# Kernel optimization log

Measured on AMD Instinct MI355X. Metric: run time of the kernel, lower is better.

## Reference

```python
import jax, jax.numpy as jnp
import numpy as np

D = 1024

def setup_inputs() -> dict:
    key = jax.random.key(0)
    ks = jax.random.split(key, 7)
    s = 1.0 / np.sqrt(D)
    x = jax.random.normal(ks[0], (4, 4096, D), dtype=jnp.float32)
    Wq = jax.random.uniform(ks[1], (D, D), jnp.float32, -s, s)
    bq = jax.random.uniform(ks[2], (D,), jnp.float32, -s, s)
    Wk = jax.random.uniform(ks[3], (D, D), jnp.float32, -s, s)
    bk = jax.random.uniform(ks[4], (D,), jnp.float32, -s, s)
    Wv = jax.random.uniform(ks[5], (D, D), jnp.float32, -s, s)
    bv = jax.random.uniform(ks[6], (D,), jnp.float32, -s, s)
    return {"x": x, "Wq": Wq, "bq": bq, "Wk": Wk, "bk": bk, "Wv": Wv, "bv": bv}

def reference(x, Wq, bq, Wk, bk, Wv, bv):
    # nn.Linear: y = x @ W.T + b
    q = (jnp.einsum('bnd,ed->bne', x, Wq) + bq) / jnp.sqrt(jnp.float32(Wq.shape[0]))
    k = jnp.einsum('bnd,ed->bne', x, Wk) + bk
    v = jnp.einsum('bnd,ed->bne', x, Wv) + bv
    scores = jnp.einsum('bqd,bkd->bqk', q, k)  # [B,N,N]
    N = scores.shape[-1]
    mask = jnp.triu(jnp.full((N, N), -1e9, dtype=scores.dtype), k=1)
    probs = jax.nn.softmax(scores + mask, axis=-1)
    return jnp.einsum('bqk,bkd->bqd', probs, v)
```

## Files before the change

kernel.cpp:

```cpp
#include <hip/hip_runtime.h>
#include <hip/hip_bf16.h>
#include <stdint.h>


typedef __attribute__((ext_vector_type(8))) short short8;
typedef __attribute__((ext_vector_type(4))) float float4v;

__device__ inline unsigned short f2b(float f) {
  union { float f; unsigned u; } v; v.f = f;
  unsigned r = (v.u + 0x7fffu + ((v.u >> 16) & 1u)) >> 16;
  return (unsigned short)r;
}
__device__ inline float b2f(unsigned short b) {
  union { unsigned u; float f; } v; v.u = ((unsigned)b) << 16;
  return v.f;
}

typedef const __attribute__((address_space(1))) unsigned int* gptr_t;
typedef __attribute__((address_space(3))) unsigned int* lptr_t;

__device__ inline void gload_lds16(const unsigned short* g, unsigned short* l) {
  __builtin_amdgcn_global_load_lds((gptr_t)(const void*)g, (lptr_t)(void*)l, 16, 0, 0);
}

__global__ __launch_bounds__(256) void cvt_all(const float* __restrict__ x,
                                               const float* __restrict__ wq,
                                               const float* __restrict__ wk,
                                               const float* __restrict__ wv,
                                               unsigned short* __restrict__ xb,
                                               unsigned short* __restrict__ wb) {
  const float* src;
  unsigned short* dst;
  long n;
  long i0;
  long stride;
  if (blockIdx.x < 2048) {
    src = x; dst = xb; n = 16384L * 1024;
    i0 = ((long)blockIdx.x * 256 + threadIdx.x) * 4;
    stride = 2048L * 256 * 4;
  } else {
    int wsec = (blockIdx.x - 2048) >> 8;
    int blk = (blockIdx.x - 2048) & 255;
    src = wsec == 0 ? wq : (wsec == 1 ? wk : wv);
    dst = wb + (long)wsec * 1024 * 1024;
    n = 1024L * 1024;
    i0 = ((long)blk * 256 + threadIdx.x) * 4;
    stride = 256L * 256 * 4;
  }
  for (long i = i0; i < n; i += stride) {
    float4 f = *(const float4*)&src[i];
    union { unsigned short u[4]; uint2 v; } o;
    o.u[0] = f2b(f.x); o.u[1] = f2b(f.y); o.u[2] = f2b(f.z); o.u[3] = f2b(f.w);
    *(uint2*)&dst[i] = o.v;
  }
}

template <int MODE>
__global__ __launch_bounds__(256) void gemm_bt(const unsigned short* __restrict__ Ag,
                                               const unsigned short* __restrict__ Bg,
                                               const float* __restrict__ b0,
                                               const float* __restrict__ b1,
                                               const float* __restrict__ b2,
                                               void* __restrict__ Cg,
                                               int N, int K,
                                               long sA, long sB, long sC) {
  const int b = blockIdx.z;
  const unsigned short* A = Ag + (long)b * sA;
  const unsigned short* B = Bg + (long)b * sB;

  int biArr[2];
  int bj;
  if (MODE == 0) {
    biArr[0] = blockIdx.x; bj = blockIdx.y;
  } else if (MODE == 1) {
    int t = blockIdx.x;
    int bi = (int)((sqrtf(8.0f * t + 1.0f) - 1.0f) * 0.5f);
    while ((bi + 1) * (bi + 2) / 2 <= t) bi++;
    while (bi * (bi + 1) / 2 > t) bi--;
    biArr[0] = bi; bj = t - bi * (bi + 1) / 2;
  } else {
    biArr[0] = blockIdx.x; biArr[1] = 31 - (int)blockIdx.x; bj = blockIdx.y;
  }

  __shared__ unsigned short As[128 * 32];
  __shared__ unsigned short Bs[128 * 32];

  const int tid = threadIdx.x;
  const int w = tid >> 6, l = tid & 63;
  const int wr = w >> 1, wc = w & 1;
  const int lr = l & 15;
  const int k8 = (l >> 4) * 8;
  const int rowB0 = bj * 128;

  const int NT = (MODE == 2) ? 2 : 1;
#pragma unroll
  for (int tt = 0; tt < NT; tt++) {
    const int bi = biArr[tt];
    const int rowA0 = bi * 128;
    int Keff = K;
    if (MODE == 2) { int cap = (bi + 1) * 128; Keff = cap < K ? cap : K; }

    float4v acc[4][4];
#pragma unroll
    for (int i = 0; i < 4; i++)
#pragma unroll
      for (int j = 0; j < 4; j++) acc[i][j] = (float4v){0.f, 0.f, 0.f, 0.f};

    for (int k0 = 0; k0 < Keff; k0 += 32) {
#pragma unroll
      for (int i = 0; i < 2; i++) {
        int c = i * 256 + tid;
        int r = c >> 2, c8 = (c & 3) * 8;
        int ldsbase = (i * 256 + w * 64) * 8;
        gload_lds16(A + (long)(rowA0 + r) * K + k0 + c8, &As[ldsbase]);
        gload_lds16(B + (long)(rowB0 + r) * K + k0 + c8, &Bs[ldsbase]);
      }
      __syncthreads();

      short8 af[4], bf[4];
#pragma unroll
      for (int mi = 0; mi < 4; mi++)
        af[mi] = *(const short8*)&As[(wr * 64 + mi * 16 + lr) * 32 + k8];
#pragma unroll
      for (int ni = 0; ni < 4; ni++)
        bf[ni] = *(const short8*)&Bs[(wc * 64 + ni * 16 + lr) * 32 + k8];
#pragma unroll
      for (int mi = 0; mi < 4; mi++)
#pragma unroll
        for (int ni = 0; ni < 4; ni++)
          acc[mi][ni] = __builtin_amdgcn_mfma_f32_16x16x32_bf16(af[mi], bf[ni], acc[mi][ni], 0, 0, 0);
      __syncthreads();
    }

    const int col0 = bj * 128 + wc * 64;
    const int row0g = bi * 128 + wr * 64;
    if (MODE == 0) {
      const int sec = bj >> 3;
      const float* bias = sec == 0 ? b0 : (sec == 1 ? b1 : b2);
      const float scale = sec == 0 ? 0.03125f : 1.0f;
      unsigned short* C = (unsigned short*)Cg + (long)sec * 16777216L;
      const int colBase = col0 - (sec << 10);
#pragma unroll
      for (int mi = 0; mi < 4; mi++) {
        int rbase = row0g + mi * 16 + (l >> 4) * 4;
#pragma unroll
        for (int ni = 0; ni < 4; ni++) {
          int col = colBase + ni * 16 + lr;
          float bvv = bias[col];
#pragma unroll
          for (int j = 0; j < 4; j++)
            C[(long)(rbase + j) * 1024 + col] = f2b((acc[mi][ni][j] + bvv) * scale);
        }
      }
    } else if (MODE == 1) {
      unsigned short* C = (unsigned short*)Cg + (long)b * sC;
#pragma unroll
      for (int mi = 0; mi < 4; mi++) {
        int rbase = row0g + mi * 16 + (l >> 4) * 4;
#pragma unroll
        for (int ni = 0; ni < 4; ni++) {
          int col = col0 + ni * 16 + lr;
#pragma unroll
          for (int j = 0; j < 4; j++)
            C[(long)(rbase + j) * N + col] = f2b(acc[mi][ni][j]);
        }
      }
    } else {
      float* C = (float*)Cg + (long)b * sC;
#pragma unroll
      for (int mi = 0; mi < 4; mi++) {
        int rbase = row0g + mi * 16 + (l >> 4) * 4;
#pragma unroll
        for (int ni = 0; ni < 4; ni++) {
          int col = col0 + ni * 16 + lr;
#pragma unroll
          for (int j = 0; j < 4; j++)
            C[(long)(rbase + j) * N + col] = acc[mi][ni][j];
        }
      }
    }
  }
}

__global__ __launch_bounds__(256) void softmax_causal(unsigned short* __restrict__ S) {
  const int bid = blockIdx.x;
  const int b = bid >> 12, i = bid & 4095;
  unsigned short* row = S + ((long)b * 4096 + i) * 4096;
  const int len = i + 1;
  const int padTo = ((i >> 7) + 1) << 7;
  const int nch = padTo >> 3;
  const int tid = threadIdx.x;
  const int w = tid >> 6;

  float v[2][8];
  int nc[2];
  float m = -3e38f;
#pragma unroll
  for (int s = 0; s < 2; s++) {
    int c = tid + s * 256;
    nc[s] = -1;
    if (c < nch) {
      nc[s] = c;
      short8 x = *(const short8*)&row[c * 8];
#pragma unroll
      for (int j = 0; j < 8; j++) {
        int idx = c * 8 + j;
        float f = (idx < len) ? b2f((unsigned short)x[j]) : -3e38f;
        v[s][j] = f;
        m = fmaxf(m, f);
      }
    }
  }

  __shared__ float red[4];
#pragma unroll
  for (int off = 32; off; off >>= 1) m = fmaxf(m, __shfl_xor(m, off));
  if ((tid & 63) == 0) red[w] = m;
  __syncthreads();
  m = fmaxf(fmaxf(red[0], red[1]), fmaxf(red[2], red[3]));

  float sum = 0.f;
#pragma unroll
  for (int s = 0; s < 2; s++) {
    if (nc[s] >= 0) {
#pragma unroll
      for (int j = 0; j < 8; j++) {
        float e = __expf(v[s][j] - m);
        v[s][j] = e;
        sum += e;
      }
    }
  }
  __syncthreads();
#pragma unroll
  for (int off = 32; off; off >>= 1) sum += __shfl_xor(sum, off);
  if ((tid & 63) == 0) red[w] = sum;
  __syncthreads();
  sum = red[0] + red[1] + red[2] + red[3];
  const float inv = 1.0f / sum;

#pragma unroll
  for (int s = 0; s < 2; s++) {
    if (nc[s] >= 0) {
      int c = nc[s];
      short8 o;
#pragma unroll
      for (int j = 0; j < 8; j++) o[j] = (short)f2b(v[s][j] * inv);
      *(short8*)&row[c * 8] = o;
    }
  }
}

__global__ __launch_bounds__(256) void transpose_v(const unsigned short* __restrict__ V,
                                                   unsigned short* __restrict__ VT) {
  __shared__ unsigned short t[64][65];
  const int b = blockIdx.z;
  const int n0 = blockIdx.x * 64;
  const int d0 = blockIdx.y * 64;
  const unsigned short* Vb = V + (long)b * 4096 * 1024;
  unsigned short* VTb = VT + (long)b * 1024 * 4096;
  const int tid = threadIdx.x;
#pragma unroll
  for (int s = 0; s < 2; s++) {
    int c = s * 256 + tid;
    int r = c >> 3, c8 = (c & 7) * 8;
    short8 x = *(const short8*)&Vb[(long)(n0 + r) * 1024 + d0 + c8];
#pragma unroll
    for (int j = 0; j < 8; j++) t[r][c8 + j] = (unsigned short)x[j];
  }
  __syncthreads();
#pragma unroll
  for (int s = 0; s < 2; s++) {
    int c = s * 256 + tid;
    int dr = c >> 3, n8 = (c & 7) * 8;
    short8 o;
#pragma unroll
    for (int j = 0; j < 8; j++) o[j] = (short)t[n8 + j][dr];
    *(short8*)&VTb[(long)(d0 + dr) * 4096 + n0 + n8] = o;
  }
}

extern "C" void kernel_launch(void* const* d_in, const int* in_sizes, int n_in,
                              void* d_out, int out_size, void* d_ws, size_t ws_size,
                              hipStream_t stream) {
  const float* x  = (const float*)d_in[0];
  const float* Wq = (const float*)d_in[1];
  const float* bq = (const float*)d_in[2];
  const float* Wk = (const float*)d_in[3];
  const float* bk = (const float*)d_in[4];
  const float* Wv = (const float*)d_in[5];
  const float* bv = (const float*)d_in[6];
  float* out = (float*)d_out;

  const long NTOK = 16384L;
  const long D = 1024L;
  const long NB = 4096L;

  unsigned short* ws = (unsigned short*)d_ws;
  unsigned short* qb = ws;
  unsigned short* kb = qb + NTOK * D;
  unsigned short* vb = kb + NTOK * D;
  unsigned short* vT = vb + NTOK * D;
  unsigned short* S  = vT + NTOK * D;
  unsigned short* xb  = S;
  unsigned short* Wb  = S + NTOK * D;

  cvt_all<<<2048 + 3 * 256, 256, 0, stream>>>(x, Wq, Wk, Wv, xb, Wb);

  gemm_bt<0><<<dim3(128, 24, 1), 256, 0, stream>>>(xb, Wb, bq, bk, bv, qb,
      1024, 1024, 0, 0, 0);

  transpose_v<<<dim3(64, 16, 4), 256, 0, stream>>>(vb, vT);

  gemm_bt<1><<<dim3(528, 1, 4), 256, 0, stream>>>(qb, kb, nullptr, nullptr, nullptr, S,
      4096, 1024, NB * D, NB * D, NB * NB);

  softmax_causal<<<16384, 256, 0, stream>>>(S);

  gemm_bt<2><<<dim3(16, 8, 4), 256, 0, stream>>>(S, vT, nullptr, nullptr, nullptr, out,
      1024, 4096, NB * NB, D * NB, NB * D);
}
```

Baseline: 539.6 us.

## Add 256x256 double-buffered swizzled GEMM for QKV projection and QK^T

Replaces the 128x128 single-stage GEMM used for the QKV projection and causal QK^T with a new 512-thread kernel. It uses 256x256 tiles and a 64-wide K tile double-buffered across 128KB of LDS, with XOR-swizzled layouts to avoid bank conflicts. Global-to-LDS loads are interleaved between MFMA quarters using explicit barriers, vmcnt waits and s_setprio, which is meant to overlap memory with compute and raise data reuse. The PV GEMM is split out unchanged. Larger tiles waste more work on diagonal blocks in the causal case, and the large LDS footprint limits occupancy.

Result: faster. 493.9 us (-8.5%).

```diff
diff --git a/kernel.cpp b/kernel.cpp
--- a/kernel.cpp
+++ b/kernel.cpp
@@ -31,9 +31,7 @@
                                                unsigned short* __restrict__ wb) {
   const float* src;
   unsigned short* dst;
-  long n;
-  long i0;
-  long stride;
+  long n, i0, stride;
   if (blockIdx.x < 2048) {
     src = x; dst = xb; n = 16384L * 1024;
     i0 = ((long)blockIdx.x * 256 + threadIdx.x) * 4;
@@ -55,32 +53,179 @@
   }
 }
 
+
+__device__ __forceinline__ void stage_half(const unsigned short* __restrict__ g,
+                                           int grow0, int tile, int kk,
+                                           char* tb, int tid) {
+  const int kc = tile * 64 + kk * 32;
+#pragma unroll
+  for (int j = 0; j < 2; j++) {
+    int c = j * 512 + tid;
+    int lc = c ^ ((c >> 3) & 3);
+    gload_lds16(g + (long)(grow0 + (lc >> 2)) * 1024 + kc + (lc & 3) * 8,
+                (unsigned short*)(tb + kk * 16384 + (j * 512 + (tid & 448)) * 16));
+  }
+}
+
+#define DSA(dst, TB, kk, mi) do { \
+  int o = (kk) * 16384 + (wr * 128 + (mi) * 16 + lr) * 64 + g16; \
+  o ^= ((o >> 3) & 0x30); dst = *(const short8*)((TB) + o); } while (0)
+#define DSB(dst, TB, kk, ni) do { \
+  int o = (kk) * 16384 + (wc * 64 + (ni) * 16 + lr) * 64 + g16; \
+  o ^= ((o >> 3) & 0x30); dst = *(const short8*)((TB) + o); } while (0)
+
+#define MF(x, y, z) __builtin_amdgcn_mfma_f32_16x16x32_bf16(x, y, z, 0, 0, 0)
+#define MMQ(M0) \
+  acc[M0 + 0][0] = MF(a0, b0, acc[M0 + 0][0]); \
+  acc[M0 + 0][1] = MF(a0, b1, acc[M0 + 0][1]); \
+  acc[M0 + 0][2] = MF(a0, b2, acc[M0 + 0][2]); \
+  acc[M0 + 0][3] = MF(a0, b3, acc[M0 + 0][3]); \
+  acc[M0 + 1][0] = MF(a1, b0, acc[M0 + 1][0]); \
+  acc[M0 + 1][1] = MF(a1, b1, acc[M0 + 1][1]); \
+  acc[M0 + 1][2] = MF(a1, b2, acc[M0 + 1][2]); \
+  acc[M0 + 1][3] = MF(a1, b3, acc[M0 + 1][3]); \
+  acc[M0 + 2][0] = MF(a2, b0, acc[M0 + 2][0]); \
+  acc[M0 + 2][1] = MF(a2, b1, acc[M0 + 2][1]); \
+  acc[M0 + 2][2] = MF(a2, b2, acc[M0 + 2][2]); \
+  acc[M0 + 2][3] = MF(a2, b3, acc[M0 + 2][3]); \
+  acc[M0 + 3][0] = MF(a3, b0, acc[M0 + 3][0]); \
+  acc[M0 + 3][1] = MF(a3, b1, acc[M0 + 3][1]); \
+  acc[M0 + 3][2] = MF(a3, b2, acc[M0 + 3][2]); \
+  acc[M0 + 3][3] = MF(a3, b3, acc[M0 + 3][3]);
+
+#define KTILE(AT, BT, OA, t) do { \
+  short8 a0, a1, a2, a3, b0, b1, b2, b3; \
+   \
+  DSB(b0, BT, 0, 0); DSB(b1, BT, 0, 1); DSB(b2, BT, 0, 2); DSB(b3, BT, 0, 3); \
+  DSA(a0, AT, 0, 0); DSA(a1, AT, 0, 1); DSA(a2, AT, 0, 2); DSA(a3, AT, 0, 3); \
+  if ((t) + 1 < NT) stage_half(A, rowA0, (t) + 1, 1, OA, tid); \
+  __builtin_amdgcn_s_barrier(); \
+  __builtin_amdgcn_s_setprio(1); MMQ(0); __builtin_amdgcn_s_setprio(0); \
+  __builtin_amdgcn_s_barrier(); \
+   \
+  DSA(a0, AT, 0, 4); DSA(a1, AT, 0, 5); DSA(a2, AT, 0, 6); DSA(a3, AT, 0, 7); \
+  if ((t) + 2 < NT) stage_half(Bm, rowB0, (t) + 2, 0, BT, tid); \
+  __builtin_amdgcn_s_barrier(); \
+  __builtin_amdgcn_s_setprio(1); MMQ(4); __builtin_amdgcn_s_setprio(0); \
+  __builtin_amdgcn_s_barrier(); \
+   \
+  DSB(b0, BT, 1, 0); DSB(b1, BT, 1, 1); DSB(b2, BT, 1, 2); DSB(b3, BT, 1, 3); \
+  DSA(a0, AT, 1, 0); DSA(a1, AT, 1, 1); DSA(a2, AT, 1, 2); DSA(a3, AT, 1, 3); \
+  if ((t) + 2 < NT) stage_half(A, rowA0, (t) + 2, 0, AT, tid); \
+  __builtin_amdgcn_s_barrier(); \
+  __builtin_amdgcn_s_setprio(1); MMQ(0); __builtin_amdgcn_s_setprio(0); \
+  __builtin_amdgcn_s_barrier(); \
+   \
+  DSA(a0, AT, 1, 4); DSA(a1, AT, 1, 5); DSA(a2, AT, 1, 6); DSA(a3, AT, 1, 7); \
+  if ((t) + 2 < NT) stage_half(Bm, rowB0, (t) + 2, 1, BT, tid); \
+  __builtin_amdgcn_s_barrier(); \
+  __builtin_amdgcn_s_setprio(1); MMQ(4); __builtin_amdgcn_s_setprio(0); \
+  if ((t) + 2 < NT) { asm volatile("s_waitcnt vmcnt(6)" ::: "memory"); } \
+  else               { asm volatile("s_waitcnt vmcnt(0)" ::: "memory"); } \
+  __builtin_amdgcn_s_barrier(); \
+} while (0)
+
 template <int MODE>
-__global__ __launch_bounds__(256) void gemm_bt(const unsigned short* __restrict__ Ag,
+__global__ __launch_bounds__(512, 2) void gemm8p(
+    const unsigned short* __restrict__ Ag, const unsigned short* __restrict__ Bg,
+    const float* __restrict__ b0v, const float* __restrict__ b1v,
+    const float* __restrict__ b2v, void* __restrict__ Cg,
+    long sA, long sB, long sC) {
+  __shared__ __align__(16) char smem[131072];
+  const int NT = 16;
+
+  int bi, bj, b;
+  if (MODE == 0) {
+    bi = blockIdx.x; bj = blockIdx.y; b = 0;
+  } else {
+    int t = blockIdx.x % 136;
+    b = blockIdx.x / 136;
+    int r = (int)((sqrtf(8.0f * t + 1.0f) - 1.0f) * 0.5f);
+    while ((r + 1) * (r + 2) / 2 <= t) r++;
+    while (r * (r + 1) / 2 > t) r--;
+    bi = r; bj = t - r * (r + 1) / 2;
+  }
+
+  const unsigned short* A = Ag + (long)b * sA;
+  const unsigned short* Bm = Bg + (long)b * sB;
+
+  const int tid = threadIdx.x;
+  const int l = tid & 63, w = tid >> 6;
+  const int wr = w >> 2, wc = w & 3;
+  const int lr = l & 15, g16 = (l >> 4) * 16;
+  const int rowA0 = bi * 256, rowB0 = bj * 256;
+
+  char* A0 = smem;
+  char* B0 = smem + 32768;
+  char* A1 = smem + 65536;
+  char* B1 = smem + 98304;
+
+  float4v acc[8][4];
+#pragma unroll
+  for (int i = 0; i < 8; i++)
+#pragma unroll
+    for (int j = 0; j < 4; j++) acc[i][j] = (float4v){0.f, 0.f, 0.f, 0.f};
+
+  stage_half(A, rowA0, 0, 0, A0, tid);
+  stage_half(Bm, rowB0, 0, 0, B0, tid);
+  stage_half(A, rowA0, 0, 1, A0, tid);
+  stage_half(Bm, rowB0, 0, 1, B0, tid);
+  stage_half(Bm, rowB0, 1, 0, B1, tid);
+  stage_half(A, rowA0, 1, 0, A1, tid);
+  stage_half(Bm, rowB0, 1, 1, B1, tid);
+  asm volatile("s_waitcnt vmcnt(6)" ::: "memory");
+  __builtin_amdgcn_s_barrier();
+
+#pragma unroll 1
+  for (int t = 0; t < NT; t += 2) {
+    KTILE(A0, B0, A1, t);
+    KTILE(A1, B1, A0, t + 1);
+  }
+
+  if (MODE == 0) {
+    const int sec = bj >> 2;
+    const float* bias = sec == 0 ? b0v : (sec == 1 ? b1v : b2v);
+    const float scale = sec == 0 ? 0.03125f : 1.0f;
+    unsigned short* C = (unsigned short*)Cg + (long)sec * 16777216L;
+    const int colbase = (bj & 3) * 256 + wc * 64;
+#pragma unroll
+    for (int mi = 0; mi < 8; mi++) {
+      int rbase = bi * 256 + wr * 128 + mi * 16 + (l >> 4) * 4;
+#pragma unroll
+      for (int ni = 0; ni < 4; ni++) {
+        int col = colbase + ni * 16 + lr;
+        float bb = bias[col];
+#pragma unroll
+        for (int j = 0; j < 4; j++)
+          C[(long)(rbase + j) * 1024 + col] = f2b((acc[mi][ni][j] + bb) * scale);
+      }
+    }
+  } else {
+    unsigned short* C = (unsigned short*)Cg + (long)b * sC;
+#pragma unroll
+    for (int mi = 0; mi < 8; mi++) {
+      int rbase = bi * 256 + wr * 128 + mi * 16 + (l >> 4) * 4;
+#pragma unroll
+      for (int ni = 0; ni < 4; ni++) {
+        int col = bj * 256 + wc * 64 + ni * 16 + lr;
+#pragma unroll
+        for (int j = 0; j < 4; j++)
+          C[(long)(rbase + j) * 4096 + col] = f2b(acc[mi][ni][j]);
+      }
+    }
+  }
+}
+
+__global__ __launch_bounds__(256) void gemm_pv(const unsigned short* __restrict__ Ag,
                                                const unsigned short* __restrict__ Bg,
-                                               const float* __restrict__ b0,
-                                               const float* __restrict__ b1,
-                                               const float* __restrict__ b2,
-                                               void* __restrict__ Cg,
+                                               float* __restrict__ Cg,
                                                int N, int K,
                                                long sA, long sB, long sC) {
   const int b = blockIdx.z;
   const unsigned short* A = Ag + (long)b * sA;
   const unsigned short* B = Bg + (long)b * sB;
-
-  int biArr[2];
-  int bj;
-  if (MODE == 0) {
-    biArr[0] = blockIdx.x; bj = blockIdx.y;
-  } else if (MODE == 1) {
-    int t = blockIdx.x;
-    int bi = (int)((sqrtf(8.0f * t + 1.0f) - 1.0f) * 0.5f);
-    while ((bi + 1) * (bi + 2) / 2 <= t) bi++;
-    while (bi * (bi + 1) / 2 > t) bi--;
-    biArr[0] = bi; bj = t - bi * (bi + 1) / 2;
-  } else {
-    biArr[0] = blockIdx.x; biArr[1] = 31 - (int)blockIdx.x; bj = blockIdx.y;
-  }
+  const int bj = blockIdx.y;
+  int biArr[2] = {(int)blockIdx.x, 31 - (int)blockIdx.x};
 
   __shared__ unsigned short As[128 * 32];
   __shared__ unsigned short Bs[128 * 32];
@@ -92,13 +237,12 @@
   const int k8 = (l >> 4) * 8;
   const int rowB0 = bj * 128;
 
-  const int NT = (MODE == 2) ? 2 : 1;
-#pragma unroll
-  for (int tt = 0; tt < NT; tt++) {
+#pragma unroll
+  for (int tt = 0; tt < 2; tt++) {
     const int bi = biArr[tt];
     const int rowA0 = bi * 128;
-    int Keff = K;
-    if (MODE == 2) { int cap = (bi + 1) * 128; Keff = cap < K ? cap : K; }
+    int cap = (bi + 1) * 128;
+    int Keff = cap < K ? cap : K;
 
     float4v acc[4][4];
 #pragma unroll
@@ -132,51 +276,18 @@
       __syncthreads();
     }
 
+    float* C = Cg + (long)b * sC;
     const int col0 = bj * 128 + wc * 64;
     const int row0g = bi * 128 + wr * 64;
-    if (MODE == 0) {
-      const int sec = bj >> 3;
-      const float* bias = sec == 0 ? b0 : (sec == 1 ? b1 : b2);
-      const float scale = sec == 0 ? 0.03125f : 1.0f;
-      unsigned short* C = (unsigned short*)Cg + (long)sec * 16777216L;
-      const int colBase = col0 - (sec << 10);
-#pragma unroll
-      for (int mi = 0; mi < 4; mi++) {
-        int rbase = row0g + mi * 16 + (l >> 4) * 4;
-#pragma unroll
-        for (int ni = 0; ni < 4; ni++) {
-          int col = colBase + ni * 16 + lr;
-          float bvv = bias[col];
-#pragma unroll
-          for (int j = 0; j < 4; j++)
-            C[(long)(rbase + j) * 1024 + col] = f2b((acc[mi][ni][j] + bvv) * scale);
-        }
-      }
-    } else if (MODE == 1) {
-      unsigned short* C = (unsigned short*)Cg + (long)b * sC;
-#pragma unroll
-      for (int mi = 0; mi < 4; mi++) {
-        int rbase = row0g + mi * 16 + (l >> 4) * 4;
-#pragma unroll
-        for (int ni = 0; ni < 4; ni++) {
-          int col = col0 + ni * 16 + lr;
-#pragma unroll
-          for (int j = 0; j < 4; j++)
-            C[(long)(rbase + j) * N + col] = f2b(acc[mi][ni][j]);
-        }
-      }
-    } else {
-      float* C = (float*)Cg + (long)b * sC;
-#pragma unroll
-      for (int mi = 0; mi < 4; mi++) {
-        int rbase = row0g + mi * 16 + (l >> 4) * 4;
-#pragma unroll
-        for (int ni = 0; ni < 4; ni++) {
-          int col = col0 + ni * 16 + lr;
-#pragma unroll
-          for (int j = 0; j < 4; j++)
-            C[(long)(rbase + j) * N + col] = acc[mi][ni][j];
-        }
+#pragma unroll
+    for (int mi = 0; mi < 4; mi++) {
+      int rbase = row0g + mi * 16 + (l >> 4) * 4;
+#pragma unroll
+      for (int ni = 0; ni < 4; ni++) {
+        int col = col0 + ni * 16 + lr;
+#pragma unroll
+        for (int j = 0; j < 4; j++)
+          C[(long)(rbase + j) * N + col] = acc[mi][ni][j];
       }
     }
   }
@@ -307,16 +418,15 @@
 
   cvt_all<<<2048 + 3 * 256, 256, 0, stream>>>(x, Wq, Wk, Wv, xb, Wb);
 
-  gemm_bt<0><<<dim3(128, 24, 1), 256, 0, stream>>>(xb, Wb, bq, bk, bv, qb,
-      1024, 1024, 0, 0, 0);
+  gemm8p<0><<<dim3(64, 12), 512, 0, stream>>>(xb, Wb, bq, bk, bv, qb, 0, 0, 0);
 
   transpose_v<<<dim3(64, 16, 4), 256, 0, stream>>>(vb, vT);
 
-  gemm_bt<1><<<dim3(528, 1, 4), 256, 0, stream>>>(qb, kb, nullptr, nullptr, nullptr, S,
-      4096, 1024, NB * D, NB * D, NB * NB);
+  gemm8p<1><<<544, 512, 0, stream>>>(qb, kb, nullptr, nullptr, nullptr, S,
+      NB * D, NB * D, NB * NB);
 
   softmax_causal<<<16384, 256, 0, stream>>>(S);
 
-  gemm_bt<2><<<dim3(16, 8, 4), 256, 0, stream>>>(S, vT, nullptr, nullptr, nullptr, out,
+  gemm_pv<<<dim3(16, 8, 4), 256, 0, stream>>>(S, vT, out,
       1024, 4096, NB * NB, D * NB, NB * D);
 }
```
